# Kernel tuning notes

Hardware: AMD Instinct MI355X
Metric: run time of the kernel (lower is better)

The kernel has to match this reference:

```python
import jax, jax.numpy as jnp
import numpy as np

TOP_K = 2

def setup_inputs() -> dict:
    key = jax.random.key(0)
    k1, k2, k3, k4, k5 = jax.random.split(key, 5)
    B, S, H, E, F = 2, 1024, 1024, 8, 2816
    scale = 0.02
    return {
        "hidden_states": jax.random.normal(k1, (B, S, H), dtype=jnp.float32),
        "gate_w": jax.random.normal(k2, (E, H), dtype=jnp.float32) * scale,
        "w1": jax.random.normal(k3, (E, H, F), dtype=jnp.float32) * scale,
        "w3": jax.random.normal(k4, (E, H, F), dtype=jnp.float32) * scale,
        "w2": jax.random.normal(k5, (E, F, H), dtype=jnp.float32) * scale,
    }

def reference(hidden_states, gate_w, w1, w3, w2):
    B, S, H = hidden_states.shape
    E = gate_w.shape[0]
    x = hidden_states.reshape(-1, H)                      # [T, H]
    T = x.shape[0]
    # Router: logits -> fp32 softmax -> top-k -> renormalize
    router_logits = jnp.einsum('th,eh->te', x, gate_w)    # [T, E]
    probs = jax.nn.softmax(router_logits.astype(jnp.float32), axis=-1)
    top_w, top_i = jax.lax.top_k(probs, TOP_K)            # [T, k]
    top_w = top_w / jnp.sum(top_w, axis=-1, keepdims=True)
    # Scatter normalized top-k weights into dense combine matrix [T, E]
    combine = jnp.zeros((T, E), dtype=probs.dtype)
    combine = combine.at[jnp.arange(T)[:, None], top_i].set(top_w)
    combine = combine.astype(x.dtype)
    # Experts: SwiGLU MLP per expert, weighted combine (dense formulation
    # of gather -> grouped GEMM -> scatter; non-selected experts get weight 0)
    g = jnp.einsum('th,ehf->tef', x, w1)                  # gate proj
    u = jnp.einsum('th,ehf->tef', x, w3)                  # up proj
    act = jax.nn.silu(g) * u                              # [T, E, F]
    act = act * combine[:, :, None]                       # apply routing weight
    out = jnp.einsum('tef,efh->th', act, w2)              # down proj + combine
    final_hidden_states = out.reshape(B, S, H)
    return final_hidden_states, router_logits
```

## Files before the change

kernel.cpp:

```cpp
#include <hip/hip_runtime.h>

typedef unsigned short u16;
typedef unsigned int u32;
typedef __attribute__((ext_vector_type(8))) short bf16x8;
typedef __attribute__((ext_vector_type(4))) float f32x4;

#define T_TOK 2048
#define H_DIM 1024
#define E_NUM 8
#define F_DIM 2816
#define BM 128
#define BN1 128
#define BN2 64
#define BK 32
#define LDK 40

__device__ __forceinline__ u16 f2bf(float f) {
    u32 b = __float_as_uint(f);
    u32 lsb = (b >> 16) & 1u;
    b += 0x7fffu + lsb;
    return (u16)(b >> 16);
}

__global__ __launch_bounds__(64) void router_kernel(
    const float* __restrict__ x, const float* __restrict__ gw,
    float* __restrict__ logits_out, int* __restrict__ cnt,
    int* __restrict__ tok_list, float* __restrict__ wt_list)
{
    int t = blockIdx.x;
    int lane = threadIdx.x;
    const float* xr = x + (size_t)t * H_DIM;

    float acc[E_NUM];
#pragma unroll
    for (int e = 0; e < E_NUM; e++) acc[e] = 0.f;

    for (int j = 0; j < H_DIM / 64; j++) {
        int idx = j * 64 + lane;
        float xv = xr[idx];
#pragma unroll
        for (int e = 0; e < E_NUM; e++)
            acc[e] += xv * gw[e * H_DIM + idx];
    }
#pragma unroll
    for (int e = 0; e < E_NUM; e++) {
        float v = acc[e];
#pragma unroll
        for (int o = 32; o > 0; o >>= 1) v += __shfl_xor(v, o, 64);
        acc[e] = v;
    }
    if (lane == 0) {
#pragma unroll
        for (int e = 0; e < E_NUM; e++) logits_out[t * E_NUM + e] = acc[e];
        float m = acc[0];
#pragma unroll
        for (int e = 1; e < E_NUM; e++) m = fmaxf(m, acc[e]);
        float p[E_NUM], s = 0.f;
#pragma unroll
        for (int e = 0; e < E_NUM; e++) { p[e] = expf(acc[e] - m); s += p[e]; }
        float inv = 1.f / s;
#pragma unroll
        for (int e = 0; e < E_NUM; e++) p[e] *= inv;
        int i0 = 0;
#pragma unroll
        for (int e = 1; e < E_NUM; e++) if (p[e] > p[i0]) i0 = e;
        int i1 = (i0 == 0) ? 1 : 0;
#pragma unroll
        for (int e = 0; e < E_NUM; e++) if (e != i0 && p[e] > p[i1]) i1 = e;
        float w0 = p[i0], w1 = p[i1];
        float rs = 1.f / (w0 + w1);
        w0 *= rs; w1 *= rs;
        int s0 = atomicAdd(&cnt[i0], 1);
        tok_list[i0 * T_TOK + s0] = t; wt_list[i0 * T_TOK + s0] = w0;
        int s1 = atomicAdd(&cnt[i1], 1);
        tok_list[i1 * T_TOK + s1] = t; wt_list[i1 * T_TOK + s1] = w1;
    }
}

__global__ void offsets_kernel(const int* __restrict__ cnt, int* __restrict__ off)
{
    if (threadIdx.x == 0 && blockIdx.x == 0) {
        int s = 0;
        for (int e = 0; e < E_NUM; e++) {
            off[e] = s;
            s += ((cnt[e] + BM - 1) / BM) * BM;
        }
    }
}

__global__ __launch_bounds__(256, 2) void gemm1_kernel(
    const float* __restrict__ x, const float* __restrict__ w1,
    const float* __restrict__ w3, const int* __restrict__ cnt,
    const int* __restrict__ off, const int* __restrict__ tok_list,
    const float* __restrict__ wt_list, u16* __restrict__ act)
{
    int e = blockIdx.z;
    int m0 = blockIdx.y * BM;
    int n0 = blockIdx.x * BN1;
    if (m0 >= cnt[e]) return;

    __shared__ __align__(16) u16 As[BM][LDK];
    __shared__ __align__(16) u16 B1[BN1][LDK];
    __shared__ __align__(16) u16 B3[BN1][LDK];
    __shared__ int tok_s[BM];
    __shared__ float wt_s[BM];

    int tid = threadIdx.x;
    if (tid < BM) {
        int tok = tok_list[e * T_TOK + m0 + tid];
        tok_s[tid] = tok;
        wt_s[tid] = (tok >= 0) ? wt_list[e * T_TOK + m0 + tid] : 0.f;
    }
    __syncthreads();

    int wid = tid >> 6, lane = tid & 63, q = lane >> 4, l15 = lane & 15;
    int wr = (wid >> 1) * 64, wc = (wid & 1) * 64;

    const f32x4 zero = {0.f, 0.f, 0.f, 0.f};
    f32x4 accg[4][4], accu[4][4];
#pragma unroll
    for (int i = 0; i < 4; i++)
#pragma unroll
        for (int j = 0; j < 4; j++) { accg[i][j] = zero; accu[i][j] = zero; }

    const int arow = tid >> 1, ah = (tid & 1) * 16;
    const int tokA = tok_s[arow];
    const int bf = tid & 127, bk0 = (tid >> 7) * 16;
    const size_t wb = (size_t)e * H_DIM * F_DIM + n0 + bf;

    for (int k0 = 0; k0 < H_DIM; k0 += BK) {
        float a16[16];
        if (tokA >= 0) {
            const float4* xr = (const float4*)(x + (size_t)tokA * H_DIM + k0 + ah);
            float4 v0 = xr[0], v1 = xr[1], v2 = xr[2], v3 = xr[3];
            a16[0]=v0.x; a16[1]=v0.y; a16[2]=v0.z;  a16[3]=v0.w;
            a16[4]=v1.x; a16[5]=v1.y; a16[6]=v1.z;  a16[7]=v1.w;
            a16[8]=v2.x; a16[9]=v2.y; a16[10]=v2.z; a16[11]=v2.w;
            a16[12]=v3.x;a16[13]=v3.y;a16[14]=v3.z; a16[15]=v3.w;
        } else {
#pragma unroll
            for (int j = 0; j < 16; j++) a16[j] = 0.f;
        }
        float b1v[16], b3v[16];
        {
            const size_t base = wb + (size_t)(k0 + bk0) * F_DIM;
#pragma unroll
            for (int j = 0; j < 16; j++) {
                b1v[j] = w1[base + (size_t)j * F_DIM];
                b3v[j] = w3[base + (size_t)j * F_DIM];
            }
        }
        __syncthreads();
        {
            union { uint4 v[2]; u16 u[16]; } pu;
#pragma unroll
            for (int j = 0; j < 16; j++) pu.u[j] = f2bf(a16[j]);
            *(uint4*)&As[arow][ah]     = pu.v[0];
            *(uint4*)&As[arow][ah + 8] = pu.v[1];
#pragma unroll
            for (int j = 0; j < 16; j++) pu.u[j] = f2bf(b1v[j]);
            *(uint4*)&B1[bf][bk0]     = pu.v[0];
            *(uint4*)&B1[bf][bk0 + 8] = pu.v[1];
#pragma unroll
            for (int j = 0; j < 16; j++) pu.u[j] = f2bf(b3v[j]);
            *(uint4*)&B3[bf][bk0]     = pu.v[0];
            *(uint4*)&B3[bf][bk0 + 8] = pu.v[1];
        }
        __syncthreads();

        bf16x8 a[4], f1[4], f3[4];
#pragma unroll
        for (int tm = 0; tm < 4; tm++)
            a[tm] = *(const bf16x8*)&As[wr + tm * 16 + l15][q * 8];
#pragma unroll
        for (int tn = 0; tn < 4; tn++) {
            f1[tn] = *(const bf16x8*)&B1[wc + tn * 16 + l15][q * 8];
            f3[tn] = *(const bf16x8*)&B3[wc + tn * 16 + l15][q * 8];
        }
#pragma unroll
        for (int tm = 0; tm < 4; tm++)
#pragma unroll
            for (int tn = 0; tn < 4; tn++) {
                accg[tm][tn] = __builtin_amdgcn_mfma_f32_16x16x32_bf16(a[tm], f1[tn], accg[tm][tn], 0, 0, 0);
                accu[tm][tn] = __builtin_amdgcn_mfma_f32_16x16x32_bf16(a[tm], f3[tn], accu[tm][tn], 0, 0, 0);
            }
    }

    const int pos0 = off[e] + m0;
#pragma unroll
    for (int tm = 0; tm < 4; tm++) {
        const int row = wr + tm * 16 + q * 4;
#pragma unroll
        for (int r = 0; r < 4; r++) {
            const float wt = wt_s[row + r];
            u16* aptr = act + (size_t)(pos0 + row + r) * F_DIM + n0 + wc + l15;
#pragma unroll
            for (int tn = 0; tn < 4; tn++) {
                float g = accg[tm][tn][r];
                float u = accu[tm][tn][r];
                float sg = g / (1.f + expf(-g));
                aptr[tn * 16] = f2bf(sg * u * wt);
            }
        }
    }
}

__global__ __launch_bounds__(256, 3) void gemm2_kernel(
    const u16* __restrict__ act, const float* __restrict__ w2,
    const int* __restrict__ cnt, const int* __restrict__ off,
    const int* __restrict__ tok_list, float* __restrict__ out)
{
    int e = blockIdx.z;
    int m0 = blockIdx.y * BM;
    int n0 = blockIdx.x * BN2;
    if (m0 >= cnt[e]) return;

    __shared__ __align__(16) u16 As[BM][LDK];
    __shared__ __align__(16) u16 Bt[BN2][LDK];
    __shared__ int tok_s[BM];

    int tid = threadIdx.x;
    if (tid < BM) tok_s[tid] = tok_list[e * T_TOK + m0 + tid];
    __syncthreads();

    int wid = tid >> 6, lane = tid & 63, q = lane >> 4, l15 = lane & 15;
    int wr = (wid >> 1) * 64, wc = (wid & 1) * 32;

    const f32x4 zero = {0.f, 0.f, 0.f, 0.f};
    f32x4 acc[4][2];
#pragma unroll
    for (int i = 0; i < 4; i++)
#pragma unroll
        for (int j = 0; j < 2; j++) acc[i][j] = zero;

    const int arow = tid >> 1, ah = (tid & 1) * 16;
    const size_t abase = (size_t)(off[e] + m0 + arow) * F_DIM + ah;
    const int bh = tid & 63, bk0 = (tid >> 6) * 8;
    const size_t wb = (size_t)e * F_DIM * H_DIM + n0 + bh;

    for (int k0 = 0; k0 < F_DIM; k0 += BK) {
        uint4 av0 = *(const uint4*)(act + abase + k0);
        uint4 av1 = *(const uint4*)(act + abase + k0 + 8);
        float bv[8];
        {
            const size_t base = wb + (size_t)(k0 + bk0) * H_DIM;
#pragma unroll
            for (int j = 0; j < 8; j++) bv[j] = w2[base + (size_t)j * H_DIM];
        }
        __syncthreads();
        *(uint4*)&As[arow][ah]     = av0;
        *(uint4*)&As[arow][ah + 8] = av1;
        {
            union { uint4 v; u16 u[8]; } pu;
#pragma unroll
            for (int j = 0; j < 8; j++) pu.u[j] = f2bf(bv[j]);
            *(uint4*)&Bt[bh][bk0] = pu.v;
        }
        __syncthreads();

        bf16x8 a[4], b[2];
#pragma unroll
        for (int tm = 0; tm < 4; tm++)
            a[tm] = *(const bf16x8*)&As[wr + tm * 16 + l15][q * 8];
#pragma unroll
        for (int tn = 0; tn < 2; tn++)
            b[tn] = *(const bf16x8*)&Bt[wc + tn * 16 + l15][q * 8];
#pragma unroll
        for (int tm = 0; tm < 4; tm++)
#pragma unroll
            for (int tn = 0; tn < 2; tn++)
                acc[tm][tn] = __builtin_amdgcn_mfma_f32_16x16x32_bf16(a[tm], b[tn], acc[tm][tn], 0, 0, 0);
    }

#pragma unroll
    for (int tm = 0; tm < 4; tm++) {
        const int row = wr + tm * 16 + q * 4;
#pragma unroll
        for (int r = 0; r < 4; r++) {
            const int tok = tok_s[row + r];
            if (tok >= 0) {
                float* optr = out + (size_t)tok * H_DIM + n0 + wc + l15;
#pragma unroll
                for (int tn = 0; tn < 2; tn++)
                    atomicAdd(&optr[tn * 16], acc[tm][tn][r]);
            }
        }
    }
}

extern "C" void kernel_launch(void* const* d_in, const int* in_sizes, int n_in,
                              void* d_out, int out_size, void* d_ws, size_t ws_size,
                              hipStream_t stream) {
    const float* x  = (const float*)d_in[0];
    const float* gw = (const float*)d_in[1];
    const float* w1 = (const float*)d_in[2];
    const float* w3 = (const float*)d_in[3];
    const float* w2 = (const float*)d_in[4];
    float* out = (float*)d_out;

    char* ws = (char*)d_ws;
    int*   cnt      = (int*)(ws);
    int*   off      = (int*)(ws + 64);
    int*   tok_list = (int*)(ws + 128);
    float* wt_list  = (float*)(ws + 128 + 65536);
    u16*   act      = (u16*)(ws + 128 + 131072);

    hipMemsetAsync(cnt, 0, 64, stream);
    hipMemsetAsync(tok_list, 0xFF, 65536, stream);
    hipMemsetAsync(out, 0, (size_t)T_TOK * H_DIM * sizeof(float), stream);

    float* logits_out = out + (size_t)T_TOK * H_DIM;
    router_kernel<<<T_TOK, 64, 0, stream>>>(x, gw, logits_out, cnt, tok_list, wt_list);
    offsets_kernel<<<1, 64, 0, stream>>>(cnt, off);
    gemm1_kernel<<<dim3(F_DIM / BN1, T_TOK / BM, E_NUM), 256, 0, stream>>>(
        x, w1, w3, cnt, off, tok_list, wt_list, act);
    gemm2_kernel<<<dim3(H_DIM / BN2, T_TOK / BM, E_NUM), 256, 0, stream>>>(
        act, w2, cnt, off, tok_list, out);
}
```

Before: 667.1 us.

## Prefetch next tiles into registers and split-K the down-projection GEMM

Both expert GEMMs now issue the global loads for the next K tile into registers before running the MFMAs on the current shared-memory tile, so memory latency overlaps with compute. The down-projection kernel doubles its K tile to 64 and splits the F dimension in two across the grid, which doubles the number of blocks. Its partial sums are combined through the existing atomic adds. The cost is more registers per thread, which can lower occupancy, and twice the atomic traffic to the output.

```diff
diff --git a/kernel.cpp b/kernel.cpp
--- a/kernel.cpp
+++ b/kernel.cpp
@@ -12,8 +12,12 @@
 #define BM 128
 #define BN1 128
 #define BN2 64
-#define BK 32
-#define LDK 40
+#define BK1 32
+#define BK2 64
+#define SPLITF 2
+#define FS (F_DIM / SPLITF)
+#define LDK1 40
+#define LDK2 72
 
 __device__ __forceinline__ u16 f2bf(float f) {
     u32 b = __float_as_uint(f);
@@ -99,9 +103,9 @@
     int n0 = blockIdx.x * BN1;
     if (m0 >= cnt[e]) return;
 
-    __shared__ __align__(16) u16 As[BM][LDK];
-    __shared__ __align__(16) u16 B1[BN1][LDK];
-    __shared__ __align__(16) u16 B3[BN1][LDK];
+    __shared__ __align__(16) u16 As[BM][LDK1];
+    __shared__ __align__(16) u16 B1[BN1][LDK1];
+    __shared__ __align__(16) u16 B3[BN1][LDK1];
     __shared__ int tok_s[BM];
     __shared__ float wt_s[BM];
 
@@ -125,48 +129,61 @@
 
     const int arow = tid >> 1, ah = (tid & 1) * 16;
     const int tokA = tok_s[arow];
+    const float* xbase = x + (tokA >= 0 ? (size_t)tokA * H_DIM + ah : 0);
     const int bf = tid & 127, bk0 = (tid >> 7) * 16;
     const size_t wb = (size_t)e * H_DIM * F_DIM + n0 + bf;
 
-    for (int k0 = 0; k0 < H_DIM; k0 += BK) {
-        float a16[16];
+    float a16[16], b1v[16], b3v[16];
+#pragma unroll
+    for (int j = 0; j < 16; j++) a16[j] = 0.f;
+
+    {
         if (tokA >= 0) {
-            const float4* xr = (const float4*)(x + (size_t)tokA * H_DIM + k0 + ah);
-            float4 v0 = xr[0], v1 = xr[1], v2 = xr[2], v3 = xr[3];
-            a16[0]=v0.x; a16[1]=v0.y; a16[2]=v0.z;  a16[3]=v0.w;
-            a16[4]=v1.x; a16[5]=v1.y; a16[6]=v1.z;  a16[7]=v1.w;
-            a16[8]=v2.x; a16[9]=v2.y; a16[10]=v2.z; a16[11]=v2.w;
-            a16[12]=v3.x;a16[13]=v3.y;a16[14]=v3.z; a16[15]=v3.w;
-        } else {
-#pragma unroll
-            for (int j = 0; j < 16; j++) a16[j] = 0.f;
-        }
-        float b1v[16], b3v[16];
+            const float4* xr = (const float4*)(xbase + 0);
+            *(float4*)&a16[0] = xr[0]; *(float4*)&a16[4] = xr[1];
+            *(float4*)&a16[8] = xr[2]; *(float4*)&a16[12] = xr[3];
+        }
+        const size_t base = wb + (size_t)bk0 * F_DIM;
+#pragma unroll
+        for (int j = 0; j < 16; j++) {
+            b1v[j] = w1[base + (size_t)j * F_DIM];
+            b3v[j] = w3[base + (size_t)j * F_DIM];
+        }
+    }
+
+    const int NIT = H_DIM / BK1;
+    for (int it = 0; it < NIT; ++it) {
         {
-            const size_t base = wb + (size_t)(k0 + bk0) * F_DIM;
+            union { uint4 v[2]; u16 u[16]; } pu;
+#pragma unroll
+            for (int j = 0; j < 16; j++) pu.u[j] = f2bf(a16[j]);
+            *(uint4*)&As[arow][ah]     = pu.v[0];
+            *(uint4*)&As[arow][ah + 8] = pu.v[1];
+#pragma unroll
+            for (int j = 0; j < 16; j++) pu.u[j] = f2bf(b1v[j]);
+            *(uint4*)&B1[bf][bk0]     = pu.v[0];
+            *(uint4*)&B1[bf][bk0 + 8] = pu.v[1];
+#pragma unroll
+            for (int j = 0; j < 16; j++) pu.u[j] = f2bf(b3v[j]);
+            *(uint4*)&B3[bf][bk0]     = pu.v[0];
+            *(uint4*)&B3[bf][bk0 + 8] = pu.v[1];
+        }
+        __syncthreads();
+
+        if (it + 1 < NIT) {
+            const int k0n = (it + 1) * BK1;
+            if (tokA >= 0) {
+                const float4* xr = (const float4*)(xbase + k0n);
+                *(float4*)&a16[0] = xr[0]; *(float4*)&a16[4] = xr[1];
+                *(float4*)&a16[8] = xr[2]; *(float4*)&a16[12] = xr[3];
+            }
+            const size_t base = wb + (size_t)(k0n + bk0) * F_DIM;
 #pragma unroll
             for (int j = 0; j < 16; j++) {
                 b1v[j] = w1[base + (size_t)j * F_DIM];
                 b3v[j] = w3[base + (size_t)j * F_DIM];
             }
         }
-        __syncthreads();
-        {
-            union { uint4 v[2]; u16 u[16]; } pu;
-#pragma unroll
-            for (int j = 0; j < 16; j++) pu.u[j] = f2bf(a16[j]);
-            *(uint4*)&As[arow][ah]     = pu.v[0];
-            *(uint4*)&As[arow][ah + 8] = pu.v[1];
-#pragma unroll
-            for (int j = 0; j < 16; j++) pu.u[j] = f2bf(b1v[j]);
-            *(uint4*)&B1[bf][bk0]     = pu.v[0];
-            *(uint4*)&B1[bf][bk0 + 8] = pu.v[1];
-#pragma unroll
-            for (int j = 0; j < 16; j++) pu.u[j] = f2bf(b3v[j]);
-            *(uint4*)&B3[bf][bk0]     = pu.v[0];
-            *(uint4*)&B3[bf][bk0 + 8] = pu.v[1];
-        }
-        __syncthreads();
 
         bf16x8 a[4], f1[4], f3[4];
 #pragma unroll
@@ -184,6 +201,7 @@
                 accg[tm][tn] = __builtin_amdgcn_mfma_f32_16x16x32_bf16(a[tm], f1[tn], accg[tm][tn], 0, 0, 0);
                 accu[tm][tn] = __builtin_amdgcn_mfma_f32_16x16x32_bf16(a[tm], f3[tn], accu[tm][tn], 0, 0, 0);
             }
+        __syncthreads();
     }
 
     const int pos0 = off[e] + m0;
@@ -210,13 +228,14 @@
     const int* __restrict__ cnt, const int* __restrict__ off,
     const int* __restrict__ tok_list, float* __restrict__ out)
 {
-    int e = blockIdx.z;
+    int e  = blockIdx.z / SPLITF;
+    int ks = blockIdx.z % SPLITF;
     int m0 = blockIdx.y * BM;
     int n0 = blockIdx.x * BN2;
     if (m0 >= cnt[e]) return;
 
-    __shared__ __align__(16) u16 As[BM][LDK];
-    __shared__ __align__(16) u16 Bt[BN2][LDK];
+    __shared__ __align__(16) u16 As[BM][LDK2];
+    __shared__ __align__(16) u16 Bt[BN2][LDK2];
     __shared__ int tok_s[BM];
 
     int tid = threadIdx.x;
@@ -233,43 +252,59 @@
 #pragma unroll
         for (int j = 0; j < 2; j++) acc[i][j] = zero;
 
-    const int arow = tid >> 1, ah = (tid & 1) * 16;
-    const size_t abase = (size_t)(off[e] + m0 + arow) * F_DIM + ah;
-    const int bh = tid & 63, bk0 = (tid >> 6) * 8;
-    const size_t wb = (size_t)e * F_DIM * H_DIM + n0 + bh;
-
-    for (int k0 = 0; k0 < F_DIM; k0 += BK) {
-        uint4 av0 = *(const uint4*)(act + abase + k0);
-        uint4 av1 = *(const uint4*)(act + abase + k0 + 8);
-        float bv[8];
+    const int arow = tid >> 1, ah = (tid & 1) * 32;
+    const u16* abase = act + (size_t)(off[e] + m0 + arow) * F_DIM + ah + (size_t)ks * FS;
+    const int bh = tid & 63, bk0 = (tid >> 6) * 16;
+    const float* wbase = w2 + (size_t)e * F_DIM * H_DIM + n0 + bh + (size_t)(ks * FS + bk0) * H_DIM;
+
+    uint4 av[4];
+    float bv[16];
+
+    {
+#pragma unroll
+        for (int j = 0; j < 4; j++) av[j] = *(const uint4*)(abase + j * 8);
+#pragma unroll
+        for (int j = 0; j < 16; j++) bv[j] = wbase[(size_t)j * H_DIM];
+    }
+
+    const int NIT = FS / BK2;
+    for (int it = 0; it < NIT; ++it) {
+#pragma unroll
+        for (int j = 0; j < 4; j++) *(uint4*)&As[arow][ah + j * 8] = av[j];
         {
-            const size_t base = wb + (size_t)(k0 + bk0) * H_DIM;
-#pragma unroll
-            for (int j = 0; j < 8; j++) bv[j] = w2[base + (size_t)j * H_DIM];
+            union { uint4 v[2]; u16 u[16]; } pu;
+#pragma unroll
+            for (int j = 0; j < 16; j++) pu.u[j] = f2bf(bv[j]);
+            *(uint4*)&Bt[bh][bk0]     = pu.v[0];
+            *(uint4*)&Bt[bh][bk0 + 8] = pu.v[1];
         }
         __syncthreads();
-        *(uint4*)&As[arow][ah]     = av0;
-        *(uint4*)&As[arow][ah + 8] = av1;
-        {
-            union { uint4 v; u16 u[8]; } pu;
-#pragma unroll
-            for (int j = 0; j < 8; j++) pu.u[j] = f2bf(bv[j]);
-            *(uint4*)&Bt[bh][bk0] = pu.v;
+
+        if (it + 1 < NIT) {
+            const int k0n = (it + 1) * BK2;
+#pragma unroll
+            for (int j = 0; j < 4; j++) av[j] = *(const uint4*)(abase + k0n + j * 8);
+            const float* wnext = wbase + (size_t)k0n * H_DIM;
+#pragma unroll
+            for (int j = 0; j < 16; j++) bv[j] = wnext[(size_t)j * H_DIM];
+        }
+
+#pragma unroll
+        for (int kk = 0; kk < 2; ++kk) {
+            bf16x8 a[4], b[2];
+#pragma unroll
+            for (int tm = 0; tm < 4; tm++)
+                a[tm] = *(const bf16x8*)&As[wr + tm * 16 + l15][kk * 32 + q * 8];
+#pragma unroll
+            for (int tn = 0; tn < 2; tn++)
+                b[tn] = *(const bf16x8*)&Bt[wc + tn * 16 + l15][kk * 32 + q * 8];
+#pragma unroll
+            for (int tm = 0; tm < 4; tm++)
+#pragma unroll
+                for (int tn = 0; tn < 2; tn++)
+                    acc[tm][tn] = __builtin_amdgcn_mfma_f32_16x16x32_bf16(a[tm], b[tn], acc[tm][tn], 0, 0, 0);
         }
         __syncthreads();
-
-        bf16x8 a[4], b[2];
-#pragma unroll
-        for (int tm = 0; tm < 4; tm++)
-            a[tm] = *(const bf16x8*)&As[wr + tm * 16 + l15][q * 8];
-#pragma unroll
-        for (int tn = 0; tn < 2; tn++)
-            b[tn] = *(const bf16x8*)&Bt[wc + tn * 16 + l15][q * 8];
-#pragma unroll
-        for (int tm = 0; tm < 4; tm++)
-#pragma unroll
-            for (int tn = 0; tn < 2; tn++)
-                acc[tm][tn] = __builtin_amdgcn_mfma_f32_16x16x32_bf16(a[tm], b[tn], acc[tm][tn], 0, 0, 0);
     }
 
 #pragma unroll
@@ -314,6 +349,6 @@
     offsets_kernel<<<1, 64, 0, stream>>>(cnt, off);
     gemm1_kernel<<<dim3(F_DIM / BN1, T_TOK / BM, E_NUM), 256, 0, stream>>>(
         x, w1, w3, cnt, off, tok_list, wt_list, act);
-    gemm2_kernel<<<dim3(H_DIM / BN2, T_TOK / BM, E_NUM), 256, 0, stream>>>(
+    gemm2_kernel<<<dim3(H_DIM / BN2, T_TOK / BM, E_NUM * SPLITF), 256, 0, stream>>>(
         act, w2, cnt, off, tok_list, out);
 }
```

Result: faster. 590.6 us (-11.5%).
